# Performance work log

Measured on AMD Instinct MI355X. Metric: run time of the kernel, lower is better.

The kernel has to match this reference:

```python
import jax, jax.numpy as jnp
import numpy as np

DPH = 64          # dim_per_head
HALF = DPH // 2   # rope half dim
NH = 8            # num heads
SCALE = jnp.sqrt(jnp.float32(DPH))


def setup_inputs() -> dict:
    key = jax.random.key(0)
    ks = jax.random.split(key, 6)
    b, H, W, d = 2, 48, 48, 512
    qk_bound = 6.0 / np.sqrt(d + DPH)
    x = jax.random.normal(ks[0], (b, H, W, d), dtype=jnp.float32)
    wq = jax.random.uniform(ks[1], (d, DPH, NH), jnp.float32, -qk_bound, qk_bound)
    wk = jax.random.uniform(ks[2], (d, DPH, NH), jnp.float32, -qk_bound, qk_bound)
    wv = jax.random.uniform(ks[3], (d, DPH, NH), jnp.float32, -qk_bound, qk_bound)
    wo = jax.random.uniform(ks[4], (d, DPH, NH), jnp.float32, -qk_bound, qk_bound)
    angles = jax.random.normal(ks[5], (2, HALF), dtype=jnp.float32)  # base_freq=1.0
    return {"x": x, "wq": wq, "wk": wk, "wv": wv, "wo": wo, "angles": angles}


def _rope_angles(H, W, angles):
    # positions: meshgrid(indexing='ij') of arange(H), arange(W) -> [H, W, 2]
    ii, jj = jnp.meshgrid(jnp.arange(H, dtype=angles.dtype),
                          jnp.arange(W, dtype=angles.dtype), indexing="ij")
    pos = jnp.stack([ii, jj], axis=-1)              # [H, W, 2]
    return jnp.einsum("ijp,pc->ijc", pos, angles)   # [H, W, HALF]


def _apply_rope(t, cos, sin):
    # t: [b, h, H, W, dv]; interleaved pairs (d c) with c=2
    tr = t.reshape(*t.shape[:-1], HALF, 2)
    t0, t1 = tr[..., 0], tr[..., 1]
    rot = jnp.stack([t0 * cos - t1 * sin, t0 * sin + t1 * cos], axis=-1)
    return rot.reshape(t.shape)


def reference(x, wq, wk, wv, wo, angles):
    b, H, W, d = x.shape
    # QKV projections: [b,H,W,d] x [d,dv,h] -> [b,h,H,W,dv]
    q = jnp.einsum("bijd,dvh->bhijv", x, wq)
    k = jnp.einsum("bijd,dvh->bhijv", x, wk)
    v = jnp.einsum("bijd,dvh->bhijv", x, wv)
    ang = _rope_angles(H, W, angles)
    cos, sin = jnp.cos(ang), jnp.sin(ang)           # [H, W, HALF]
    q = _apply_rope(q, cos, sin)
    k = _apply_rope(k, cos, sin)
    # flatten spatial dims -> sequence
    n = H * W
    qf = q.reshape(b, NH, n, DPH)
    kf = k.reshape(b, NH, n, DPH)
    vf = v.reshape(b, NH, n, DPH)
    scores = jnp.einsum("bhqd,bhkd->bhqk", qf, kf) / SCALE
    attn = jax.nn.softmax(scores, axis=-1)
    out = jnp.einsum("bhqk,bhkd->bhqd", attn, vf).reshape(b, NH, H, W, DPH)
    # out projection: [b,h,H,W,dv] x [d,dv,h] -> [b,H,W,d]
    return jnp.einsum("bhijv,dvh->bijd", out, wo)
```

## Files before the change

kernel.cpp:

```cpp
#include <hip/hip_runtime.h>
#include <hip/hip_bf16.h>
#include <math.h>

#define BB   2
#define WW   48
#define DD   512
#define DPH  64
#define NHH  8
#define NSEQ 2304
#define NPOS (BB*NSEQ)
#define NXE  (NPOS*DD)
#define WSZ  (DD*DD)
#define NROWS (BB*NHH*NSEQ)

typedef __attribute__((ext_vector_type(8))) short short8v;
typedef __attribute__((ext_vector_type(4))) float f32x4;

__device__ __forceinline__ ushort f2bf(float f) {
    union { __hip_bfloat16 h; ushort u; } cv;
    cv.h = __float2bfloat16(f);
    return cv.u;
}
__device__ __forceinline__ float bf2f(ushort u) {
    return __uint_as_float(((uint)u) << 16);
}
__device__ __forceinline__ uint pack2bf(float lo, float hi) {
    return (uint)f2bf(lo) | ((uint)f2bf(hi) << 16);
}
__device__ __forceinline__ float fexp2(float x) {
#if __has_builtin(__builtin_amdgcn_exp2f)
    return __builtin_amdgcn_exp2f(x);
#else
    return exp2f(x);
#endif
}
#define QSCL (0.125f * 1.44269504088896f)

__global__ __launch_bounds__(256) void k_prep(
    const float* __restrict__ x,  const float* __restrict__ wq,
    const float* __restrict__ wk, const float* __restrict__ wv,
    const float* __restrict__ wo,
    ushort* __restrict__ xh, ushort* __restrict__ xl,
    ushort* __restrict__ Bqh, ushort* __restrict__ Bql,
    ushort* __restrict__ Bkh, ushort* __restrict__ Bkl,
    ushort* __restrict__ Bvh, ushort* __restrict__ Bvl,
    ushort* __restrict__ Boh, ushort* __restrict__ Bol)
{
    int idx = blockIdx.x*256 + threadIdx.x;
    float s;
    ushort *ph, *pl; int o;
    if (idx < NXE) {
        s = x[idx]; ph = xh; pl = xl; o = idx;
    } else {
        int t = idx - NXE;
        int sel = t >> 18;
        o = t & (WSZ-1);
        int c = o >> 9, k = o & 511;
        if (sel == 0)      { s = wq[k*512 + c] * QSCL;   ph = Bqh; pl = Bql; }
        else if (sel == 1) { s = wk[k*512 + c];          ph = Bkh; pl = Bkl; }
        else if (sel == 2) { s = wv[k*512 + c];          ph = Bvh; pl = Bvl; }
        else               { s = wo[c*512 + ((k&63)<<3) + (k>>6)]; ph = Boh; pl = Bol; }
    }
    ushort hi = f2bf(s);
    ph[o] = hi;
    pl[o] = f2bf(s - bf2f(hi));
}

#define LPITCH 80
__global__ __launch_bounds__(256) void k_gemm_qkv(
    const ushort* __restrict__ xhp, const ushort* __restrict__ xlp,
    const ushort* __restrict__ Bqh, const ushort* __restrict__ Bql,
    const ushort* __restrict__ Bkh, const ushort* __restrict__ Bkl,
    const ushort* __restrict__ Bvh, const ushort* __restrict__ Bvl,
    const float* __restrict__ ang,
    ushort* __restrict__ qa, ushort* __restrict__ ka, ushort* __restrict__ vT)
{
    __shared__ char xsh[64*LPITCH], xsl[64*LPITCH];
    __shared__ char wsh[128*LPITCH], wsl[128*LPITCH];
    const int tid = threadIdx.x;
    const int w = tid>>6, l = tid&63, g = l>>4, lr = l&15;
    const int mid = blockIdx.x / 288;
    const int rmb = blockIdx.x - mid*288;
    const int rowblk = rmb >> 2, colblk = rmb & 3;
    const int row0 = rowblk*64, col0 = colblk*128;
    const ushort* Bh; const ushort* Bl;
    if (mid==0)      { Bh = Bqh; Bl = Bql; }
    else if (mid==1) { Bh = Bkh; Bl = Bkl; }
    else             { Bh = Bvh; Bl = Bvl; }

    f32x4 acc[4][2];
#pragma unroll
    for (int mt=0;mt<4;++mt)
#pragma unroll
        for (int nt=0;nt<2;++nt) acc[mt][nt] = (f32x4){0.f,0.f,0.f,0.f};

#pragma unroll 1
    for (int kc = 0; kc < 16; ++kc) {
        const int k0 = kc*32;
        __syncthreads();
#pragma unroll
        for (int u = 0; u < 2; ++u) {
            int i2 = tid + 256*u;
            int tile = i2 >> 8, t2 = i2 & 255;
            int sr = t2 >> 2, sg = t2 & 3;
            const ushort* src = (tile ? xlp : xhp) + (size_t)(row0+sr)*512 + k0 + sg*8;
            char* dst = (tile ? xsl : xsh) + sr*LPITCH + sg*16;
            *reinterpret_cast<uint4*>(dst) = *reinterpret_cast<const uint4*>(src);
        }
#pragma unroll
        for (int u = 0; u < 4; ++u) {
            int i2 = tid + 256*u;
            int tile = i2 >> 9, t2 = i2 & 511;
            int c = t2 >> 2, sg = t2 & 3;
            const ushort* src = (tile ? Bl : Bh) + (size_t)(col0+c)*512 + k0 + sg*8;
            char* dst = (tile ? wsl : wsh) + c*LPITCH + sg*16;
            *reinterpret_cast<uint4*>(dst) = *reinterpret_cast<const uint4*>(src);
        }
        __syncthreads();
        short8v ah[4], al[4], bh_[2], bl_[2];
#pragma unroll
        for (int mt = 0; mt < 4; ++mt) {
            ah[mt] = *reinterpret_cast<const short8v*>(xsh + (mt*16+lr)*LPITCH + g*16);
            al[mt] = *reinterpret_cast<const short8v*>(xsl + (mt*16+lr)*LPITCH + g*16);
        }
#pragma unroll
        for (int nt = 0; nt < 2; ++nt) {
            bh_[nt] = *reinterpret_cast<const short8v*>(wsh + (w*32+nt*16+lr)*LPITCH + g*16);
            bl_[nt] = *reinterpret_cast<const short8v*>(wsl + (w*32+nt*16+lr)*LPITCH + g*16);
        }
#pragma unroll
        for (int mt = 0; mt < 4; ++mt)
#pragma unroll
            for (int nt = 0; nt < 2; ++nt) {
                acc[mt][nt] = __builtin_amdgcn_mfma_f32_16x16x32_bf16(ah[mt], bh_[nt], acc[mt][nt], 0, 0, 0);
                acc[mt][nt] = __builtin_amdgcn_mfma_f32_16x16x32_bf16(ah[mt], bl_[nt], acc[mt][nt], 0, 0, 0);
                acc[mt][nt] = __builtin_amdgcn_mfma_f32_16x16x32_bf16(al[mt], bh_[nt], acc[mt][nt], 0, 0, 0);
            }
    }

    const int b = row0 / NSEQ;
    const int rem0 = row0 - b*NSEQ;
    if (mid < 2) {
        ushort* dst = (mid==0) ? qa : ka;
        const int sgn = (lr >= 8);
#pragma unroll
        for (int nt = 0; nt < 2; ++nt) {
            int cbase = col0 + w*32 + nt*16;
            int pc = cbase >> 4;
            float a_i = ang[pc], a_j = ang[32 + pc];
            int c = cbase + lr;
            int h = c & 7, v = c >> 3;
            ushort* colbase = dst + ((size_t)(b*NHH + h)*NSEQ)*DPH + v;
#pragma unroll
            for (int mt = 0; mt < 4; ++mt)
#pragma unroll
                for (int r = 0; r < 4; ++r) {
                    int rowrem = rem0 + mt*16 + 4*g + r;
                    int i = rowrem / WW, j = rowrem - (rowrem/WW)*WW;
                    float th = (float)i*a_i + (float)j*a_j;
                    float sn, cn; __sincosf(th, &sn, &cn);
                    float own = acc[mt][nt][r];
                    float oth = __shfl_xor(own, 8);
                    float rot = sgn ? (oth*sn + own*cn) : (own*cn - oth*sn);
                    colbase[(size_t)rowrem*DPH] = f2bf(rot);
                }
        }
    } else {
#pragma unroll
        for (int nt = 0; nt < 2; ++nt) {
            int c = col0 + w*32 + nt*16 + lr;
            int h = c & 7, v = c >> 3;
            ushort* colbase = vT + ((size_t)((b*NHH + h)*DPH + v))*NSEQ + rem0;
#pragma unroll
            for (int mt = 0; mt < 4; ++mt)
#pragma unroll
                for (int r = 0; r < 4; ++r)
                    colbase[mt*16 + 4*g + r] = f2bf(acc[mt][nt][r]);
        }
    }
}

__global__ __launch_bounds__(256) void k_gemm_o(
    const ushort* __restrict__ Oa, const ushort* __restrict__ Boh,
    const ushort* __restrict__ Bol, float* __restrict__ out)
{
    __shared__ char xs[64*LPITCH];
    __shared__ char wsh[128*LPITCH], wsl[128*LPITCH];
    const int tid = threadIdx.x;
    const int w = tid>>6, l = tid&63, g = l>>4, lr = l&15;
    const int row0 = (blockIdx.x >> 2)*64;
    const int col0 = (blockIdx.x & 3)*128;

    f32x4 acc[4][2];
#pragma unroll
    for (int mt=0;mt<4;++mt)
#pragma unroll
        for (int nt=0;nt<2;++nt) acc[mt][nt] = (f32x4){0.f,0.f,0.f,0.f};

#pragma unroll 1
    for (int kc = 0; kc < 16; ++kc) {
        const int k0 = kc*32;
        __syncthreads();
        {
            int sr = tid >> 2, sg = tid & 3;
            *reinterpret_cast<uint4*>(xs + sr*LPITCH + sg*16) =
                *reinterpret_cast<const uint4*>(Oa + (size_t)(row0+sr)*512 + k0 + sg*8);
        }
#pragma unroll
        for (int u = 0; u < 4; ++u) {
            int i2 = tid + 256*u;
            int tile = i2 >> 9, t2 = i2 & 511;
            int c = t2 >> 2, sg = t2 & 3;
            const ushort* src = (tile ? Bol : Boh) + (size_t)(col0+c)*512 + k0 + sg*8;
            char* dst = (tile ? wsl : wsh) + c*LPITCH + sg*16;
            *reinterpret_cast<uint4*>(dst) = *reinterpret_cast<const uint4*>(src);
        }
        __syncthreads();
        short8v a[4], bh_[2], bl_[2];
#pragma unroll
        for (int mt = 0; mt < 4; ++mt)
            a[mt] = *reinterpret_cast<const short8v*>(xs + (mt*16+lr)*LPITCH + g*16);
#pragma unroll
        for (int nt = 0; nt < 2; ++nt) {
            bh_[nt] = *reinterpret_cast<const short8v*>(wsh + (w*32+nt*16+lr)*LPITCH + g*16);
            bl_[nt] = *reinterpret_cast<const short8v*>(wsl + (w*32+nt*16+lr)*LPITCH + g*16);
        }
#pragma unroll
        for (int mt = 0; mt < 4; ++mt)
#pragma unroll
            for (int nt = 0; nt < 2; ++nt) {
                acc[mt][nt] = __builtin_amdgcn_mfma_f32_16x16x32_bf16(a[mt], bh_[nt], acc[mt][nt], 0, 0, 0);
                acc[mt][nt] = __builtin_amdgcn_mfma_f32_16x16x32_bf16(a[mt], bl_[nt], acc[mt][nt], 0, 0, 0);
            }
    }

#pragma unroll
    for (int mt=0;mt<4;++mt)
#pragma unroll
        for (int r=0;r<4;++r) {
            float* rowp = out + (size_t)(row0 + mt*16 + 4*g + r)*DD + col0 + w*32;
#pragma unroll
            for (int nt=0;nt<2;++nt)
                rowp[nt*16 + lr] = acc[mt][nt][r];
        }
}

#define CK 64
#define KP 72
__global__ __launch_bounds__(256) void k_attn_mfma(
    const ushort* __restrict__ qb, const ushort* __restrict__ kb,
    const ushort* __restrict__ vb, ushort* __restrict__ Op,
    float2* __restrict__ mlp)
{
    __shared__ ushort ksm[CK][KP];
    __shared__ ushort vsm[CK][KP];
    __shared__ ushort psm[4][16][KP];
    const int tid = threadIdx.x;
    const int w = tid >> 6, l = tid & 63;
    const int g = l >> 4, lr = l & 15;
    const int sp  = blockIdx.x / 576;
    const int rest = blockIdx.x - sp*576;
    const int bh = rest / 36;
    const int qc = rest - bh*36;
    const int row0 = qc * 64;
    const ushort* kbase = kb + (size_t)bh*NSEQ*DPH;
    const ushort* vbase = vb + (size_t)bh*DPH*NSEQ;

    const ushort* qptr = qb + ((size_t)bh*NSEQ + row0 + 16*w + lr)*DPH + g*8;
    const short8v qB0 = *reinterpret_cast<const short8v*>(qptr);
    const short8v qB1 = *reinterpret_cast<const short8v*>(qptr + 32);

    float m_ln = -INFINITY, l_ln = 0.f;
    f32x4 o[4];
#pragma unroll
    for (int vt = 0; vt < 4; ++vt) o[vt] = (f32x4){0.f,0.f,0.f,0.f};

    for (int t = sp*18; t < sp*18 + 18; ++t) {
        __syncthreads();
#pragma unroll
        for (int i = 0; i < 2; ++i) {
            int tau = tid + 256*i;
            int row = tau >> 3, cg = tau & 7;
            *reinterpret_cast<uint4*>(&ksm[row][cg*8]) =
                *reinterpret_cast<const uint4*>(kbase + ((size_t)(t*CK + row))*DPH + cg*8);
            *reinterpret_cast<uint4*>(&vsm[row][cg*8]) =
                *reinterpret_cast<const uint4*>(vbase + (size_t)row*NSEQ + t*CK + cg*8);
        }
        __syncthreads();

        f32x4 sc[4];
#pragma unroll
        for (int tile = 0; tile < 4; ++tile) {
            short8v k0 = *reinterpret_cast<const short8v*>(&ksm[tile*16 + lr][g*8]);
            short8v k1 = *reinterpret_cast<const short8v*>(&ksm[tile*16 + lr][32 + g*8]);
            f32x4 a2 = (f32x4){0.f,0.f,0.f,0.f};
            a2 = __builtin_amdgcn_mfma_f32_16x16x32_bf16(k0, qB0, a2, 0, 0, 0);
            a2 = __builtin_amdgcn_mfma_f32_16x16x32_bf16(k1, qB1, a2, 0, 0, 0);
            sc[tile] = a2;
        }

        float cm = sc[0][0];
#pragma unroll
        for (int tile = 0; tile < 4; ++tile)
#pragma unroll
            for (int r = 0; r < 4; ++r)
                cm = fmaxf(cm, sc[tile][r]);
        cm = fmaxf(cm, __shfl_xor(cm, 16));
        cm = fmaxf(cm, __shfl_xor(cm, 32));
        float mn = fmaxf(m_ln, cm);
        float f = fexp2(m_ln - mn);
        m_ln = mn;
        float rs = 0.f;
#pragma unroll
        for (int tile = 0; tile < 4; ++tile)
#pragma unroll
            for (int r = 0; r < 4; ++r) {
                float p = fexp2(sc[tile][r] - mn);
                sc[tile][r] = p;
                rs += p;
            }
        rs += __shfl_xor(rs, 16);
        rs += __shfl_xor(rs, 32);
        l_ln = l_ln*f + rs;

#pragma unroll
        for (int tile = 0; tile < 4; ++tile) {
            uint2 pk;
            pk.x = pack2bf(sc[tile][0], sc[tile][1]);
            pk.y = pack2bf(sc[tile][2], sc[tile][3]);
            *reinterpret_cast<uint2*>(&psm[w][lr][16*tile + 4*g]) = pk;
        }

        float f4[4];
#pragma unroll
        for (int r = 0; r < 4; ++r)
            f4[r] = __shfl(f, 4*g + r, 16);
#pragma unroll
        for (int vt = 0; vt < 4; ++vt)
#pragma unroll
            for (int r = 0; r < 4; ++r)
                o[vt][r] *= f4[r];

#pragma unroll
        for (int half = 0; half < 2; ++half) {
            short8v pA = *reinterpret_cast<const short8v*>(&psm[w][lr][32*half + g*8]);
#pragma unroll
            for (int vt = 0; vt < 4; ++vt) {
                short8v vf = *reinterpret_cast<const short8v*>(&vsm[vt*16 + lr][32*half + g*8]);
                o[vt] = __builtin_amdgcn_mfma_f32_16x16x32_bf16(pA, vf, o[vt], 0, 0, 0);
            }
        }
    }

    ushort* obase = Op + ((size_t)sp*NROWS + (size_t)bh*NSEQ + row0 + 16*w)*64;
#pragma unroll
    for (int vt = 0; vt < 4; ++vt)
#pragma unroll
        for (int r = 0; r < 4; ++r)
            obase[(4*g + r)*64 + vt*16 + lr] = f2bf(o[vt][r]);
    if (g == 0)
        mlp[sp*NROWS + bh*NSEQ + row0 + 16*w + lr] = make_float2(m_ln, l_ln);
}

__global__ __launch_bounds__(256) void k_combine(
    const ushort* __restrict__ Op, const float2* __restrict__ mlp,
    ushort* __restrict__ Oa)
{
    const int tid = threadIdx.x;
    const int row = blockIdx.x*32 + (tid >> 3);
    const int c8 = (tid & 7)*8;
    float2 a = mlp[row], b = mlp[NROWS + row];
    float M = fmaxf(a.x, b.x);
    float w0 = fexp2(a.x - M), w1 = fexp2(b.x - M);
    float inv = 1.f / (a.y*w0 + b.y*w1);
    const ushort* p0 = Op + (size_t)row*64 + c8;
    const ushort* p1 = p0 + (size_t)NROWS*64;
    uint4 u0 = *reinterpret_cast<const uint4*>(p0);
    uint4 u1 = *reinterpret_cast<const uint4*>(p1);
    const ushort* s0 = reinterpret_cast<const ushort*>(&u0);
    const ushort* s1 = reinterpret_cast<const ushort*>(&u1);
    ushort res[8];
#pragma unroll
    for (int i = 0; i < 8; ++i)
        res[i] = f2bf((bf2f(s0[i])*w0 + bf2f(s1[i])*w1) * inv);
    int bh = row / NSEQ, n = row - bh*NSEQ;
    int b_ = bh >> 3, h_ = bh & 7;
    ushort* dst = Oa + ((size_t)(b_*NSEQ + n))*DD + h_*64 + c8;
    *reinterpret_cast<uint4*>(dst) = *reinterpret_cast<const uint4*>(res);
}

extern "C" void kernel_launch(void* const* d_in, const int* in_sizes, int n_in,
                              void* d_out, int out_size, void* d_ws, size_t ws_size,
                              hipStream_t stream) {
    const float* x   = (const float*)d_in[0];
    const float* wq  = (const float*)d_in[1];
    const float* wk  = (const float*)d_in[2];
    const float* wv  = (const float*)d_in[3];
    const float* wo  = (const float*)d_in[4];
    const float* ang = (const float*)d_in[5];
    float* out = (float*)d_out;

    ushort* xh  = (ushort*)d_ws;
    ushort* xl  = xh + NXE;
    ushort* Bqh = xl + NXE;
    ushort* Bql = Bqh + WSZ;
    ushort* Bkh = Bql + WSZ;
    ushort* Bkl = Bkh + WSZ;
    ushort* Bvh = Bkl + WSZ;
    ushort* Bvl = Bvh + WSZ;
    ushort* Boh = Bvl + WSZ;
    ushort* Bol = Boh + WSZ;
    ushort* qa  = Bol + WSZ;
    ushort* ka  = qa + NXE;
    ushort* vT  = ka + NXE;
    ushort* Oa  = vT + NXE;
    ushort* Op  = xh;
    float2* mlp = (float2*)Bqh;

    k_prep<<<(NXE + 4*WSZ)/256, 256, 0, stream>>>(x, wq, wk, wv, wo,
        xh, xl, Bqh, Bql, Bkh, Bkl, Bvh, Bvl, Boh, Bol);
    k_gemm_qkv<<<864, 256, 0, stream>>>(xh, xl, Bqh, Bql, Bkh, Bkl, Bvh, Bvl,
        ang, qa, ka, vT);
    k_attn_mfma<<<1152, 256, 0, stream>>>(qa, ka, vT, Op, mlp);
    k_combine<<<NROWS/32, 256, 0, stream>>>(Op, mlp, Oa);
    k_gemm_o<<<288, 256, 0, stream>>>(Oa, Boh, Bol, out);
}
```

Before: 198.8 us.

## Fuse split-KV combine into output GEMM and reorder QKV weight columns for coalesced stores

```diff
diff --git a/kernel.cpp b/kernel.cpp
--- a/kernel.cpp
+++ b/kernel.cpp
@@ -56,9 +56,10 @@
         int sel = t >> 18;
         o = t & (WSZ-1);
         int c = o >> 9, k = o & 511;
-        if (sel == 0)      { s = wq[k*512 + c] * QSCL;   ph = Bqh; pl = Bql; }
-        else if (sel == 1) { s = wk[k*512 + c];          ph = Bkh; pl = Bkl; }
-        else if (sel == 2) { s = wv[k*512 + c];          ph = Bvh; pl = Bvl; }
+        int widx = k*512 + ((c & 63) << 3) + (c >> 6);
+        if (sel == 0)      { s = wq[widx] * QSCL; ph = Bqh; pl = Bql; }
+        else if (sel == 1) { s = wk[widx];        ph = Bkh; pl = Bkl; }
+        else if (sel == 2) { s = wv[widx];        ph = Bvh; pl = Bvl; }
         else               { s = wo[c*512 + ((k&63)<<3) + (k>>6)]; ph = Boh; pl = Bol; }
     }
     ushort hi = f2bf(s);
@@ -75,8 +76,11 @@
     const float* __restrict__ ang,
     ushort* __restrict__ qa, ushort* __restrict__ ka, ushort* __restrict__ vT)
 {
-    __shared__ char xsh[64*LPITCH], xsl[64*LPITCH];
-    __shared__ char wsh[128*LPITCH], wsl[128*LPITCH];
+    __shared__ char smem[30720];
+    char* xsh = smem;
+    char* xsl = smem + 5120;
+    char* wsh = smem + 10240;
+    char* wsl = smem + 20480;
     const int tid = threadIdx.x;
     const int w = tid>>6, l = tid&63, g = l>>4, lr = l&15;
     const int mid = blockIdx.x / 288;
@@ -142,15 +146,12 @@
     const int rem0 = row0 - b*NSEQ;
     if (mid < 2) {
         ushort* dst = (mid==0) ? qa : ka;
-        const int sgn = (lr >= 8);
+        const int odd = lr & 1;
 #pragma unroll
         for (int nt = 0; nt < 2; ++nt) {
-            int cbase = col0 + w*32 + nt*16;
-            int pc = cbase >> 4;
+            int c = col0 + w*32 + nt*16 + lr;
+            int pc = (c & 63) >> 1;
             float a_i = ang[pc], a_j = ang[32 + pc];
-            int c = cbase + lr;
-            int h = c & 7, v = c >> 3;
-            ushort* colbase = dst + ((size_t)(b*NHH + h)*NSEQ)*DPH + v;
 #pragma unroll
             for (int mt = 0; mt < 4; ++mt)
 #pragma unroll
@@ -160,29 +161,38 @@
                     float th = (float)i*a_i + (float)j*a_j;
                     float sn, cn; __sincosf(th, &sn, &cn);
                     float own = acc[mt][nt][r];
-                    float oth = __shfl_xor(own, 8);
-                    float rot = sgn ? (oth*sn + own*cn) : (own*cn - oth*sn);
-                    colbase[(size_t)rowrem*DPH] = f2bf(rot);
+                    float oth = __shfl_xor(own, 1);
+                    float rot = odd ? (oth*sn + own*cn) : (own*cn - oth*sn);
+                    dst[(size_t)(b*NSEQ + rowrem)*DD + c] = f2bf(rot);
                 }
         }
     } else {
+        __syncthreads();
+        ushort (*tile)[72] = reinterpret_cast<ushort(*)[72]>(smem);
 #pragma unroll
         for (int nt = 0; nt < 2; ++nt) {
-            int c = col0 + w*32 + nt*16 + lr;
-            int h = c & 7, v = c >> 3;
-            ushort* colbase = vT + ((size_t)((b*NHH + h)*DPH + v))*NSEQ + rem0;
+            int cl = w*32 + nt*16 + lr;
 #pragma unroll
             for (int mt = 0; mt < 4; ++mt)
 #pragma unroll
                 for (int r = 0; r < 4; ++r)
-                    colbase[mt*16 + 4*g + r] = f2bf(acc[mt][nt][r]);
+                    tile[cl][mt*16 + 4*g + r] = f2bf(acc[mt][nt][r]);
+        }
+        __syncthreads();
+        int col = tid >> 1, half = tid & 1;
+        ushort* dst = vT + ((size_t)(b*DD + col0 + col))*NSEQ + rem0 + half*32;
+#pragma unroll
+        for (int q2 = 0; q2 < 4; ++q2) {
+            uint4 val = *reinterpret_cast<const uint4*>(&tile[col][half*32 + q2*8]);
+            *reinterpret_cast<uint4*>(dst + q2*8) = val;
         }
     }
 }
 
 __global__ __launch_bounds__(256) void k_gemm_o(
-    const ushort* __restrict__ Oa, const ushort* __restrict__ Boh,
-    const ushort* __restrict__ Bol, float* __restrict__ out)
+    const ushort* __restrict__ Op, const float2* __restrict__ mlp,
+    const ushort* __restrict__ Boh, const ushort* __restrict__ Bol,
+    float* __restrict__ out)
 {
     __shared__ char xs[64*LPITCH];
     __shared__ char wsh[128*LPITCH], wsl[128*LPITCH];
@@ -190,6 +200,8 @@
     const int w = tid>>6, l = tid&63, g = l>>4, lr = l&15;
     const int row0 = (blockIdx.x >> 2)*64;
     const int col0 = (blockIdx.x & 3)*128;
+    const int b = row0 / NSEQ;
+    const int rem0 = row0 - b*NSEQ;
 
     f32x4 acc[4][2];
 #pragma unroll
@@ -203,8 +215,24 @@
         __syncthreads();
         {
             int sr = tid >> 2, sg = tid & 3;
+            int h = kc >> 1;
+            int vv = (kc & 1)*32 + sg*8;
+            size_t arow = (size_t)(b*NHH + h)*NSEQ + rem0 + sr;
+            float2 a0 = mlp[arow], a1 = mlp[NROWS + arow];
+            float M = fmaxf(a0.x, a1.x);
+            float w0 = fexp2(a0.x - M), w1 = fexp2(a1.x - M);
+            float inv = 1.f / (a0.y*w0 + a1.y*w1);
+            w0 *= inv; w1 *= inv;
+            uint4 u0 = *reinterpret_cast<const uint4*>(Op + arow*64 + vv);
+            uint4 u1 = *reinterpret_cast<const uint4*>(Op + ((size_t)NROWS + arow)*64 + vv);
+            const ushort* s0 = reinterpret_cast<const ushort*>(&u0);
+            const ushort* s1 = reinterpret_cast<const ushort*>(&u1);
+            ushort res[8];
+#pragma unroll
+            for (int i2 = 0; i2 < 8; ++i2)
+                res[i2] = f2bf(bf2f(s0[i2])*w0 + bf2f(s1[i2])*w1);
             *reinterpret_cast<uint4*>(xs + sr*LPITCH + sg*16) =
-                *reinterpret_cast<const uint4*>(Oa + (size_t)(row0+sr)*512 + k0 + sg*8);
+                *reinterpret_cast<const uint4*>(res);
         }
 #pragma unroll
         for (int u = 0; u < 4; ++u) {
@@ -263,10 +291,11 @@
     const int bh = rest / 36;
     const int qc = rest - bh*36;
     const int row0 = qc * 64;
-    const ushort* kbase = kb + (size_t)bh*NSEQ*DPH;
-    const ushort* vbase = vb + (size_t)bh*DPH*NSEQ;
-
-    const ushort* qptr = qb + ((size_t)bh*NSEQ + row0 + 16*w + lr)*DPH + g*8;
+    const int b_ = bh >> 3, h_ = bh & 7;
+    const ushort* kbase = kb + (size_t)b_*NSEQ*DD + h_*64;
+    const ushort* vbase = vb + ((size_t)(b_*DD + h_*64))*NSEQ;
+
+    const ushort* qptr = qb + ((size_t)(b_*NSEQ) + row0 + 16*w + lr)*DD + h_*64 + g*8;
     const short8v qB0 = *reinterpret_cast<const short8v*>(qptr);
     const short8v qB1 = *reinterpret_cast<const short8v*>(qptr + 32);
 
@@ -282,7 +311,7 @@
             int tau = tid + 256*i;
             int row = tau >> 3, cg = tau & 7;
             *reinterpret_cast<uint4*>(&ksm[row][cg*8]) =
-                *reinterpret_cast<const uint4*>(kbase + ((size_t)(t*CK + row))*DPH + cg*8);
+                *reinterpret_cast<const uint4*>(kbase + ((size_t)(t*CK + row))*DD + cg*8);
             *reinterpret_cast<uint4*>(&vsm[row][cg*8]) =
                 *reinterpret_cast<const uint4*>(vbase + (size_t)row*NSEQ + t*CK + cg*8);
         }
@@ -360,33 +389,6 @@
             obase[(4*g + r)*64 + vt*16 + lr] = f2bf(o[vt][r]);
     if (g == 0)
         mlp[sp*NROWS + bh*NSEQ + row0 + 16*w + lr] = make_float2(m_ln, l_ln);
-}
-
-__global__ __launch_bounds__(256) void k_combine(
-    const ushort* __restrict__ Op, const float2* __restrict__ mlp,
-    ushort* __restrict__ Oa)
-{
-    const int tid = threadIdx.x;
-    const int row = blockIdx.x*32 + (tid >> 3);
-    const int c8 = (tid & 7)*8;
-    float2 a = mlp[row], b = mlp[NROWS + row];
-    float M = fmaxf(a.x, b.x);
-    float w0 = fexp2(a.x - M), w1 = fexp2(b.x - M);
-    float inv = 1.f / (a.y*w0 + b.y*w1);
-    const ushort* p0 = Op + (size_t)row*64 + c8;
-    const ushort* p1 = p0 + (size_t)NROWS*64;
-    uint4 u0 = *reinterpret_cast<const uint4*>(p0);
-    uint4 u1 = *reinterpret_cast<const uint4*>(p1);
-    const ushort* s0 = reinterpret_cast<const ushort*>(&u0);
-    const ushort* s1 = reinterpret_cast<const ushort*>(&u1);
-    ushort res[8];
-#pragma unroll
-    for (int i = 0; i < 8; ++i)
-        res[i] = f2bf((bf2f(s0[i])*w0 + bf2f(s1[i])*w1) * inv);
-    int bh = row / NSEQ, n = row - bh*NSEQ;
-    int b_ = bh >> 3, h_ = bh & 7;
-    ushort* dst = Oa + ((size_t)(b_*NSEQ + n))*DD + h_*64 + c8;
-    *reinterpret_cast<uint4*>(dst) = *reinterpret_cast<const uint4*>(res);
 }
 
 extern "C" void kernel_launch(void* const* d_in, const int* in_sizes, int n_in,
@@ -413,7 +415,6 @@
     ushort* qa  = Bol + WSZ;
     ushort* ka  = qa + NXE;
     ushort* vT  = ka + NXE;
-    ushort* Oa  = vT + NXE;
     ushort* Op  = xh;
     float2* mlp = (float2*)Bqh;
 
@@ -422,6 +423,5 @@
     k_gemm_qkv<<<864, 256, 0, stream>>>(xh, xl, Bqh, Bql, Bkh, Bkl, Bvh, Bvl,
         ang, qa, ka, vT);
     k_attn_mfma<<<1152, 256, 0, stream>>>(qa, ka, vT, Op, mlp);
-    k_combine<<<NROWS/32, 256, 0, stream>>>(Op, mlp, Oa);
-    k_gemm_o<<<288, 256, 0, stream>>>(Oa, Boh, Bol, out);
-}
+    k_gemm_o<<<288, 256, 0, stream>>>(Op, mlp, Boh, Bol, out);
+}
```

Result: faster. 192.4 us (-3.2%).
